# Kernel tuning notes

Hardware: AMD Instinct MI355X
Metric: run time of the kernel (lower is better)

The kernel has to match this reference:

```python
import jax, jax.numpy as jnp
import numpy as np

SCALE = 0.08838834764831845  # 1/sqrt(128)


def setup_inputs() -> dict:
    key = jax.random.key(0)
    k1, k2, k3, k4 = jax.random.split(key, 4)
    B, Sq, H, D = 1, 2048, 32, 128
    Skv, K = 4096, 256
    return {
        "q": jax.random.normal(k1, (B, Sq, H, D), jnp.float32),
        "kv": jax.random.normal(k2, (B, Skv, 2, D), jnp.float32),  # stacked K,V (MQA)
        "attn_sink": jax.random.normal(k3, (H,), jnp.float32),
        "topk_idxs": jax.random.randint(k4, (B, Sq, K), 0, Skv),
    }


def reference(q, kv, attn_sink, topk_idxs):
    # q:        [B, Sq, H, D]
    # kv:       [B, Skv, 2, D]  (index 0 = keys, 1 = values; shared across heads)
    # topk_idxs:[B, Sq, K]      per-query selected KV positions
    # attn_sink:[H]             per-head sink logit added to the softmax denominator
    B = q.shape[0]
    # Gather selected KV per query: [B, Sq, K, 2, D]
    gathered = kv[jnp.arange(B)[:, None, None], topk_idxs]
    k = gathered[..., 0, :]  # [B, Sq, K, D]
    v = gathered[..., 1, :]  # [B, Sq, K, D]

    scores = jnp.einsum("bqhd,bqkd->bqhk", q, k) * SCALE  # [B, Sq, H, K]
    sink = attn_sink[None, None, :, None]                  # [1, 1, H, 1]

    # Numerically stable softmax over K selected tokens + sink logit.
    m = jnp.maximum(jnp.max(scores, axis=-1, keepdims=True), sink)
    e = jnp.exp(scores - m)
    denom = jnp.sum(e, axis=-1, keepdims=True) + jnp.exp(sink - m)
    probs = e / denom                                      # sink absorbs leftover mass

    out = jnp.einsum("bqhk,bqkd->bqhd", probs, v)          # [B, Sq, H, D]
    return out
```

## Files before the change

### kernel.cpp

```cpp
#include <hip/hip_runtime.h>
#include <hip/hip_bf16.h>

#define SQ 2048
#define NH 32
#define DH 128
#define NK 256
#define SCALE 0.08838834764831845f
#define LOG2E 1.4426950408889634f

typedef __attribute__((ext_vector_type(8))) __bf16 bf16x8;
typedef __attribute__((ext_vector_type(4))) float floatx4;

#define QS_STRIDE 136
#define KS_STRIDE 136
#define VB_STRIDE 72
#define PB_STRIDE 264

#define OFF_KV   16896
#define OFF_TOPK 35328
#define OFF_SINK 36352
#define OFF_RED  36480
#define OFF_RED2 36992
#define SMEM_SZ  37504

__device__ __forceinline__ unsigned pk_bf16(float a, float b) {
  union { __hip_bfloat162 h2; unsigned u; } c;
  c.h2 = __float22bfloat162_rn(make_float2(a, b));
  return c.u;
}

__device__ __forceinline__ float fast_exp2(float x) {
#if __has_builtin(__builtin_amdgcn_exp2f)
  return __builtin_amdgcn_exp2f(x);
#else
  return exp2f(x);
#endif
}

template <int CTRL>
__device__ __forceinline__ float dpp_rot(float x) {
  int i = __builtin_bit_cast(int, x);
  i = __builtin_amdgcn_mov_dpp(i, CTRL, 0xF, 0xF, true);
  return __builtin_bit_cast(float, i);
}
#define RED16_MAX(v) { v = fmaxf(v, dpp_rot<0x121>(v)); v = fmaxf(v, dpp_rot<0x122>(v)); \
                       v = fmaxf(v, dpp_rot<0x124>(v)); v = fmaxf(v, dpp_rot<0x128>(v)); }
#define RED16_SUM(v) { v += dpp_rot<0x121>(v); v += dpp_rot<0x122>(v); \
                       v += dpp_rot<0x124>(v); v += dpp_rot<0x128>(v); }

__global__ __launch_bounds__(256) void kv_to_bf16(const float* __restrict__ kv,
                                                  unsigned short* __restrict__ kvb) {
  int i = blockIdx.x * 256 + threadIdx.x;
  float4 f = ((const float4*)kv)[i];
  uint2 o = { pk_bf16(f.x, f.y), pk_bf16(f.z, f.w) };
  ((uint2*)kvb)[i] = o;
}

struct KR { uint4 v[4]; };
struct VR { uint4 a, b, c, d; };

__device__ __forceinline__ KR k_load(const unsigned short* __restrict__ kvb,
                                     const int* __restrict__ tks, int c, int tid) {
  int r = tid >> 2, seg = tid & 3;
  int idx = tks[c * 64 + r];
  const uint4* p = (const uint4*)(kvb + (size_t)idx * 256 + seg * 32);
  KR k;
#pragma unroll
  for (int i = 0; i < 4; i++) k.v[i] = p[i];
  return k;
}

__device__ __forceinline__ void k_write(unsigned short* kvbuf, const KR& k, int tid) {
  int r = tid >> 2, seg = tid & 3;
  uint4* d = (uint4*)&kvbuf[r * KS_STRIDE + seg * 32];
#pragma unroll
  for (int i = 0; i < 4; i++) d[i] = k.v[i];
}

__device__ __forceinline__ VR v_load(const unsigned short* __restrict__ kvb,
                                     const int* tks, int c, int tid) {
  int rg = tid & 15, dg = tid >> 4;
  int r0 = rg * 4, d0 = dg * 8;
  int4 i4 = *(const int4*)&tks[c * 64 + r0];
  VR v;
  v.a = *(const uint4*)(kvb + (size_t)i4.x * 256 + 128 + d0);
  v.b = *(const uint4*)(kvb + (size_t)i4.y * 256 + 128 + d0);
  v.c = *(const uint4*)(kvb + (size_t)i4.z * 256 + 128 + d0);
  v.d = *(const uint4*)(kvb + (size_t)i4.w * 256 + 128 + d0);
  return v;
}

__device__ __forceinline__ void v_write(unsigned short* kvbuf, const VR& v, int tid) {
  int rg = tid & 15, dg = tid >> 4;
  int r0 = rg * 4, d0 = dg * 8;
  const unsigned* pa = (const unsigned*)&v.a;
  const unsigned* pb = (const unsigned*)&v.b;
  const unsigned* pc = (const unsigned*)&v.c;
  const unsigned* pd = (const unsigned*)&v.d;
#pragma unroll
  for (int w = 0; w < 4; w++) {
    unsigned lo01 = __builtin_amdgcn_perm(pb[w], pa[w], 0x05040100u);
    unsigned lo23 = __builtin_amdgcn_perm(pd[w], pc[w], 0x05040100u);
    unsigned hi01 = __builtin_amdgcn_perm(pb[w], pa[w], 0x07060302u);
    unsigned hi23 = __builtin_amdgcn_perm(pd[w], pc[w], 0x07060302u);
    uint2 lo = { lo01, lo23 }, hi = { hi01, hi23 };
    *(uint2*)&kvbuf[(d0 + 2 * w) * VB_STRIDE + r0] = lo;
    *(uint2*)&kvbuf[(d0 + 2 * w + 1) * VB_STRIDE + r0] = hi;
  }
}

__device__ __forceinline__ void gemm1(const unsigned short* kvbuf,
                                      const bf16x8 af[2][4], int nrow, int quad,
                                      floatx4& a0, floatx4& a1) {
  a0 = (floatx4){0.f, 0.f, 0.f, 0.f};
  a1 = (floatx4){0.f, 0.f, 0.f, 0.f};
#pragma unroll
  for (int ks = 0; ks < 4; ks++) {
    bf16x8 b = *(const bf16x8*)&kvbuf[nrow * KS_STRIDE + ks * 32 + quad * 8];
    a0 = __builtin_amdgcn_mfma_f32_16x16x32_bf16(af[0][ks], b, a0, 0, 0, 0);
    a1 = __builtin_amdgcn_mfma_f32_16x16x32_bf16(af[1][ks], b, a1, 0, 0, 0);
  }
}

__device__ __forceinline__ void pv_chunk(const unsigned short* pbuf,
                                         const unsigned short* kvbuf, int c,
                                         int wave, int quad, int l16,
                                         floatx4 oacc[2][2]) {
#pragma unroll
  for (int ks = 0; ks < 2; ks++) {
    int kof = c * 64 + ks * 32 + quad * 8;
    bf16x8 a0 = *(const bf16x8*)&pbuf[l16 * PB_STRIDE + kof];
    bf16x8 a1 = *(const bf16x8*)&pbuf[(16 + l16) * PB_STRIDE + kof];
    int kl = ks * 32 + quad * 8;
    bf16x8 b0 = *(const bf16x8*)&kvbuf[(wave * 32 + l16) * VB_STRIDE + kl];
    bf16x8 b1 = *(const bf16x8*)&kvbuf[(wave * 32 + 16 + l16) * VB_STRIDE + kl];
    oacc[0][0] = __builtin_amdgcn_mfma_f32_16x16x32_bf16(a0, b0, oacc[0][0], 0, 0, 0);
    oacc[0][1] = __builtin_amdgcn_mfma_f32_16x16x32_bf16(a0, b1, oacc[0][1], 0, 0, 0);
    oacc[1][0] = __builtin_amdgcn_mfma_f32_16x16x32_bf16(a1, b0, oacc[1][0], 0, 0, 0);
    oacc[1][1] = __builtin_amdgcn_mfma_f32_16x16x32_bf16(a1, b1, oacc[1][1], 0, 0, 0);
  }
}

__global__ __launch_bounds__(256, 4) void sparse_attn_kernel(
    const float* __restrict__ q, const unsigned short* __restrict__ kvb,
    const float* __restrict__ sink, const int* __restrict__ topk,
    float* __restrict__ out) {
  __shared__ __align__(16) char smem[SMEM_SZ];
  unsigned short* qs    = (unsigned short*)smem;
  unsigned short* pbuf  = (unsigned short*)smem;
  unsigned short* kvbuf = (unsigned short*)(smem + OFF_KV);
  int*   topk_s = (int*)(smem + OFF_TOPK);
  float* sink_s = (float*)(smem + OFF_SINK);
  float* red    = (float*)(smem + OFF_RED);
  float* red2   = (float*)(smem + OFF_RED2);

  const int tid = threadIdx.x;
  const int s = blockIdx.x;
  const int wave = tid >> 6;
  const int lane = tid & 63;
  const int quad = lane >> 4;
  const int l16 = lane & 15;
  const int* tkg = topk + (size_t)s * NK;

  topk_s[tid] = tkg[tid];
  if (tid < 32) sink_s[tid] = sink[tid] * LOG2E;
  {
    int r = tid >> 2, seg = tid & 3;
    int idx = tkg[r];
    const uint4* p = (const uint4*)(kvb + (size_t)idx * 256 + seg * 32);
    uint4* d = (uint4*)&kvbuf[r * KS_STRIDE + seg * 32];
#pragma unroll
    for (int i = 0; i < 4; i++) d[i] = p[i];
  }
  {
    const float QSC = SCALE * LOG2E;
    const float* qp = q + (size_t)s * (NH * DH);
    int h = tid >> 3, d0 = (tid & 7) * 16;
    const float4* src = (const float4*)(qp + h * DH + d0);
    float4 f0 = src[0], f1 = src[1], f2 = src[2], f3 = src[3];
    uint4 o0 = { pk_bf16(f0.x * QSC, f0.y * QSC), pk_bf16(f0.z * QSC, f0.w * QSC),
                 pk_bf16(f1.x * QSC, f1.y * QSC), pk_bf16(f1.z * QSC, f1.w * QSC) };
    uint4 o1 = { pk_bf16(f2.x * QSC, f2.y * QSC), pk_bf16(f2.z * QSC, f2.w * QSC),
                 pk_bf16(f3.x * QSC, f3.y * QSC), pk_bf16(f3.z * QSC, f3.w * QSC) };
    *(uint4*)&qs[h * QS_STRIDE + d0] = o0;
    *(uint4*)&qs[h * QS_STRIDE + d0 + 8] = o1;
  }
  KR k1 = k_load(kvb, tkg, 1, tid);
  __syncthreads();

  bf16x8 afrag[2][4];
#pragma unroll
  for (int mt = 0; mt < 2; mt++)
#pragma unroll
    for (int ks = 0; ks < 4; ks++)
      afrag[mt][ks] =
          *(const bf16x8*)&qs[(mt * 16 + l16) * QS_STRIDE + ks * 32 + quad * 8];

  const int nrow = wave * 16 + l16;

  floatx4 sc[4][2];
  gemm1(kvbuf, afrag, nrow, quad, sc[0][0], sc[0][1]);
  __syncthreads();
  k_write(kvbuf, k1, tid);
  KR k2 = k_load(kvb, topk_s, 2, tid);
  __syncthreads();

  gemm1(kvbuf, afrag, nrow, quad, sc[1][0], sc[1][1]);
  __syncthreads();
  k_write(kvbuf, k2, tid);
  KR k3 = k_load(kvb, topk_s, 3, tid);
  __syncthreads();

  gemm1(kvbuf, afrag, nrow, quad, sc[2][0], sc[2][1]);
  __syncthreads();
  k_write(kvbuf, k3, tid);
  VR v0 = v_load(kvb, topk_s, 0, tid);
  __syncthreads();

  gemm1(kvbuf, afrag, nrow, quad, sc[3][0], sc[3][1]);
  __syncthreads();
  v_write(kvbuf, v0, tid);
  VR v1 = v_load(kvb, topk_s, 1, tid);

  float mh[2][4];
#pragma unroll
  for (int mt = 0; mt < 2; mt++)
#pragma unroll
    for (int r = 0; r < 4; r++) {
      float v = fmaxf(fmaxf(sc[0][mt][r], sc[1][mt][r]),
                      fmaxf(sc[2][mt][r], sc[3][mt][r]));
      RED16_MAX(v);
      mh[mt][r] = v;
    }
  if (l16 == 0) {
#pragma unroll
    for (int mt = 0; mt < 2; mt++)
#pragma unroll
      for (int r = 0; r < 4; r++)
        red[wave * 32 + mt * 16 + quad * 4 + r] = mh[mt][r];
  }
  __syncthreads();
#pragma unroll
  for (int mt = 0; mt < 2; mt++)
#pragma unroll
    for (int r = 0; r < 4; r++) {
      int h = mt * 16 + quad * 4 + r;
      float v = sink_s[h];
#pragma unroll
      for (int w = 0; w < 4; w++) v = fmaxf(v, red[w * 32 + h]);
      mh[mt][r] = v;
    }
  float ps[2][4];
#pragma unroll
  for (int mt = 0; mt < 2; mt++)
#pragma unroll
    for (int r = 0; r < 4; r++) {
      float acc = 0.f;
#pragma unroll
      for (int c = 0; c < 4; c++) {
        float e = fast_exp2(sc[c][mt][r] - mh[mt][r]);
        sc[c][mt][r] = e;
        acc += e;
      }
      RED16_SUM(acc);
      ps[mt][r] = acc;
    }
  if (l16 == 0) {
#pragma unroll
    for (int mt = 0; mt < 2; mt++)
#pragma unroll
      for (int r = 0; r < 4; r++)
        red2[wave * 32 + mt * 16 + quad * 4 + r] = ps[mt][r];
  }
  __syncthreads();
  float inv[2][4];
#pragma unroll
  for (int mt = 0; mt < 2; mt++)
#pragma unroll
    for (int r = 0; r < 4; r++) {
      int h = mt * 16 + quad * 4 + r;
      float dd = fast_exp2(sink_s[h] - mh[mt][r]);
#pragma unroll
      for (int w = 0; w < 4; w++) dd += red2[w * 32 + h];
      inv[mt][r] = 1.0f / dd;
    }
#pragma unroll
  for (int c = 0; c < 4; c++)
#pragma unroll
    for (int mt = 0; mt < 2; mt++) {
      int col = c * 64 + wave * 16 + l16;
      unsigned short* pb = &pbuf[(mt * 16 + quad * 4) * PB_STRIDE + col];
      unsigned p01 = pk_bf16(sc[c][mt][0], sc[c][mt][1]);
      unsigned p23 = pk_bf16(sc[c][mt][2], sc[c][mt][3]);
      pb[0] = (unsigned short)p01;
      pb[PB_STRIDE] = (unsigned short)(p01 >> 16);
      pb[2 * PB_STRIDE] = (unsigned short)p23;
      pb[3 * PB_STRIDE] = (unsigned short)(p23 >> 16);
    }
  __syncthreads();

  floatx4 oacc[2][2];
#pragma unroll
  for (int mt = 0; mt < 2; mt++)
#pragma unroll
    for (int nt = 0; nt < 2; nt++)
      oacc[mt][nt] = (floatx4){0.f, 0.f, 0.f, 0.f};

  pv_chunk(pbuf, kvbuf, 0, wave, quad, l16, oacc);
  __syncthreads();
  v_write(kvbuf, v1, tid);
  VR v2 = v_load(kvb, topk_s, 2, tid);
  __syncthreads();

  pv_chunk(pbuf, kvbuf, 1, wave, quad, l16, oacc);
  __syncthreads();
  v_write(kvbuf, v2, tid);
  VR v3 = v_load(kvb, topk_s, 3, tid);
  __syncthreads();

  pv_chunk(pbuf, kvbuf, 2, wave, quad, l16, oacc);
  __syncthreads();
  v_write(kvbuf, v3, tid);
  __syncthreads();

  pv_chunk(pbuf, kvbuf, 3, wave, quad, l16, oacc);

  {
    float* op = out + (size_t)s * (NH * DH);
#pragma unroll
    for (int mt = 0; mt < 2; mt++)
#pragma unroll
      for (int nt = 0; nt < 2; nt++)
#pragma unroll
        for (int r4 = 0; r4 < 4; r4++) {
          int h = mt * 16 + quad * 4 + r4;
          int d = wave * 32 + nt * 16 + l16;
          op[h * DH + d] = oacc[mt][nt][r4] * inv[mt][r4];
        }
  }
}

extern "C" void kernel_launch(void* const* d_in, const int* in_sizes, int n_in,
                              void* d_out, int out_size, void* d_ws, size_t ws_size,
                              hipStream_t stream) {
  (void)in_sizes; (void)n_in; (void)out_size; (void)ws_size;
  const float* q    = (const float*)d_in[0];
  const float* kv   = (const float*)d_in[1];
  const float* sink = (const float*)d_in[2];
  const int*   topk = (const int*)d_in[3];
  float* out = (float*)d_out;
  unsigned short* kvb = (unsigned short*)d_ws;

  kv_to_bf16<<<dim3(1024), dim3(256), 0, stream>>>(kv, kvb);
  sparse_attn_kernel<<<dim3(SQ), dim3(256), 0, stream>>>(q, kvb, sink, topk, out);
}
```

Before: 113.4 us.

## Load K and Q MFMA fragments directly from global, drop LDS staging for QK

```diff
diff --git a/kernel.cpp b/kernel.cpp
--- a/kernel.cpp
+++ b/kernel.cpp
@@ -11,17 +11,14 @@
 typedef __attribute__((ext_vector_type(8))) __bf16 bf16x8;
 typedef __attribute__((ext_vector_type(4))) float floatx4;
 
-#define QS_STRIDE 136
-#define KS_STRIDE 136
 #define VB_STRIDE 72
 #define PB_STRIDE 264
 
-#define OFF_KV   16896
-#define OFF_TOPK 35328
-#define OFF_SINK 36352
-#define OFF_RED  36480
-#define OFF_RED2 36992
-#define SMEM_SZ  37504
+#define OFF_VB   16896
+#define OFF_SINK 35328
+#define OFF_RED  35456
+#define OFF_RED2 35968
+#define SMEM_SZ  36480
 
 __device__ __forceinline__ unsigned pk_bf16(float a, float b) {
   union { __hip_bfloat162 h2; unsigned u; } c;
@@ -56,32 +53,13 @@
   ((uint2*)kvb)[i] = o;
 }
 
-struct KR { uint4 v[4]; };
 struct VR { uint4 a, b, c, d; };
 
-__device__ __forceinline__ KR k_load(const unsigned short* __restrict__ kvb,
-                                     const int* __restrict__ tks, int c, int tid) {
-  int r = tid >> 2, seg = tid & 3;
-  int idx = tks[c * 64 + r];
-  const uint4* p = (const uint4*)(kvb + (size_t)idx * 256 + seg * 32);
-  KR k;
-#pragma unroll
-  for (int i = 0; i < 4; i++) k.v[i] = p[i];
-  return k;
-}
-
-__device__ __forceinline__ void k_write(unsigned short* kvbuf, const KR& k, int tid) {
-  int r = tid >> 2, seg = tid & 3;
-  uint4* d = (uint4*)&kvbuf[r * KS_STRIDE + seg * 32];
-#pragma unroll
-  for (int i = 0; i < 4; i++) d[i] = k.v[i];
-}
-
-__device__ __forceinline__ VR v_load(const unsigned short* __restrict__ kvb,
-                                     const int* tks, int c, int tid) {
+__device__ __forceinline__ VR v_load_g(const unsigned short* __restrict__ kvb,
+                                       const int* __restrict__ tkg, int c, int tid) {
   int rg = tid & 15, dg = tid >> 4;
   int r0 = rg * 4, d0 = dg * 8;
-  int4 i4 = *(const int4*)&tks[c * 64 + r0];
+  int4 i4 = *(const int4*)(tkg + c * 64 + r0);
   VR v;
   v.a = *(const uint4*)(kvb + (size_t)i4.x * 256 + 128 + d0);
   v.b = *(const uint4*)(kvb + (size_t)i4.y * 256 + 128 + d0);
@@ -90,7 +68,7 @@
   return v;
 }
 
-__device__ __forceinline__ void v_write(unsigned short* kvbuf, const VR& v, int tid) {
+__device__ __forceinline__ void v_write(unsigned short* vbuf, const VR& v, int tid) {
   int rg = tid & 15, dg = tid >> 4;
   int r0 = rg * 4, d0 = dg * 8;
   const unsigned* pa = (const unsigned*)&v.a;
@@ -104,26 +82,13 @@
     unsigned hi01 = __builtin_amdgcn_perm(pb[w], pa[w], 0x07060302u);
     unsigned hi23 = __builtin_amdgcn_perm(pd[w], pc[w], 0x07060302u);
     uint2 lo = { lo01, lo23 }, hi = { hi01, hi23 };
-    *(uint2*)&kvbuf[(d0 + 2 * w) * VB_STRIDE + r0] = lo;
-    *(uint2*)&kvbuf[(d0 + 2 * w + 1) * VB_STRIDE + r0] = hi;
-  }
-}
-
-__device__ __forceinline__ void gemm1(const unsigned short* kvbuf,
-                                      const bf16x8 af[2][4], int nrow, int quad,
-                                      floatx4& a0, floatx4& a1) {
-  a0 = (floatx4){0.f, 0.f, 0.f, 0.f};
-  a1 = (floatx4){0.f, 0.f, 0.f, 0.f};
-#pragma unroll
-  for (int ks = 0; ks < 4; ks++) {
-    bf16x8 b = *(const bf16x8*)&kvbuf[nrow * KS_STRIDE + ks * 32 + quad * 8];
-    a0 = __builtin_amdgcn_mfma_f32_16x16x32_bf16(af[0][ks], b, a0, 0, 0, 0);
-    a1 = __builtin_amdgcn_mfma_f32_16x16x32_bf16(af[1][ks], b, a1, 0, 0, 0);
+    *(uint2*)&vbuf[(d0 + 2 * w) * VB_STRIDE + r0] = lo;
+    *(uint2*)&vbuf[(d0 + 2 * w + 1) * VB_STRIDE + r0] = hi;
   }
 }
 
 __device__ __forceinline__ void pv_chunk(const unsigned short* pbuf,
-                                         const unsigned short* kvbuf, int c,
+                                         const unsigned short* vbuf, int c,
                                          int wave, int quad, int l16,
                                          floatx4 oacc[2][2]) {
 #pragma unroll
@@ -132,8 +97,8 @@
     bf16x8 a0 = *(const bf16x8*)&pbuf[l16 * PB_STRIDE + kof];
     bf16x8 a1 = *(const bf16x8*)&pbuf[(16 + l16) * PB_STRIDE + kof];
     int kl = ks * 32 + quad * 8;
-    bf16x8 b0 = *(const bf16x8*)&kvbuf[(wave * 32 + l16) * VB_STRIDE + kl];
-    bf16x8 b1 = *(const bf16x8*)&kvbuf[(wave * 32 + 16 + l16) * VB_STRIDE + kl];
+    bf16x8 b0 = *(const bf16x8*)&vbuf[(wave * 32 + l16) * VB_STRIDE + kl];
+    bf16x8 b1 = *(const bf16x8*)&vbuf[(wave * 32 + 16 + l16) * VB_STRIDE + kl];
     oacc[0][0] = __builtin_amdgcn_mfma_f32_16x16x32_bf16(a0, b0, oacc[0][0], 0, 0, 0);
     oacc[0][1] = __builtin_amdgcn_mfma_f32_16x16x32_bf16(a0, b1, oacc[0][1], 0, 0, 0);
     oacc[1][0] = __builtin_amdgcn_mfma_f32_16x16x32_bf16(a1, b0, oacc[1][0], 0, 0, 0);
@@ -146,10 +111,8 @@
     const float* __restrict__ sink, const int* __restrict__ topk,
     float* __restrict__ out) {
   __shared__ __align__(16) char smem[SMEM_SZ];
-  unsigned short* qs    = (unsigned short*)smem;
-  unsigned short* pbuf  = (unsigned short*)smem;
-  unsigned short* kvbuf = (unsigned short*)(smem + OFF_KV);
-  int*   topk_s = (int*)(smem + OFF_TOPK);
+  unsigned short* pbuf = (unsigned short*)smem;
+  unsigned short* vbuf = (unsigned short*)(smem + OFF_VB);
   float* sink_s = (float*)(smem + OFF_SINK);
   float* red    = (float*)(smem + OFF_RED);
   float* red2   = (float*)(smem + OFF_RED2);
@@ -161,66 +124,53 @@
   const int quad = lane >> 4;
   const int l16 = lane & 15;
   const int* tkg = topk + (size_t)s * NK;
-
-  topk_s[tid] = tkg[tid];
+  const float QSC = SCALE * LOG2E;
+
   if (tid < 32) sink_s[tid] = sink[tid] * LOG2E;
-  {
-    int r = tid >> 2, seg = tid & 3;
-    int idx = tkg[r];
-    const uint4* p = (const uint4*)(kvb + (size_t)idx * 256 + seg * 32);
-    uint4* d = (uint4*)&kvbuf[r * KS_STRIDE + seg * 32];
-#pragma unroll
-    for (int i = 0; i < 4; i++) d[i] = p[i];
-  }
-  {
-    const float QSC = SCALE * LOG2E;
-    const float* qp = q + (size_t)s * (NH * DH);
-    int h = tid >> 3, d0 = (tid & 7) * 16;
-    const float4* src = (const float4*)(qp + h * DH + d0);
-    float4 f0 = src[0], f1 = src[1], f2 = src[2], f3 = src[3];
-    uint4 o0 = { pk_bf16(f0.x * QSC, f0.y * QSC), pk_bf16(f0.z * QSC, f0.w * QSC),
-                 pk_bf16(f1.x * QSC, f1.y * QSC), pk_bf16(f1.z * QSC, f1.w * QSC) };
-    uint4 o1 = { pk_bf16(f2.x * QSC, f2.y * QSC), pk_bf16(f2.z * QSC, f2.w * QSC),
-                 pk_bf16(f3.x * QSC, f3.y * QSC), pk_bf16(f3.z * QSC, f3.w * QSC) };
-    *(uint4*)&qs[h * QS_STRIDE + d0] = o0;
-    *(uint4*)&qs[h * QS_STRIDE + d0 + 8] = o1;
-  }
-  KR k1 = k_load(kvb, tkg, 1, tid);
-  __syncthreads();
+
+  int kidx[4];
+#pragma unroll
+  for (int c = 0; c < 4; c++) kidx[c] = tkg[c * 64 + wave * 16 + l16];
 
   bf16x8 afrag[2][4];
 #pragma unroll
   for (int mt = 0; mt < 2; mt++)
 #pragma unroll
-    for (int ks = 0; ks < 4; ks++)
-      afrag[mt][ks] =
-          *(const bf16x8*)&qs[(mt * 16 + l16) * QS_STRIDE + ks * 32 + quad * 8];
-
-  const int nrow = wave * 16 + l16;
+    for (int ks = 0; ks < 4; ks++) {
+      const float4* p = (const float4*)(q + (size_t)s * (NH * DH) +
+                                        (mt * 16 + l16) * DH + ks * 32 + quad * 8);
+      float4 f0 = p[0], f1 = p[1];
+      union { uint4 u; bf16x8 h; } cv;
+      cv.u = (uint4){ pk_bf16(f0.x, f0.y), pk_bf16(f0.z, f0.w),
+                      pk_bf16(f1.x, f1.y), pk_bf16(f1.z, f1.w) };
+      afrag[mt][ks] = cv.h;
+    }
 
   floatx4 sc[4][2];
-  gemm1(kvbuf, afrag, nrow, quad, sc[0][0], sc[0][1]);
-  __syncthreads();
-  k_write(kvbuf, k1, tid);
-  KR k2 = k_load(kvb, topk_s, 2, tid);
-  __syncthreads();
-
-  gemm1(kvbuf, afrag, nrow, quad, sc[1][0], sc[1][1]);
-  __syncthreads();
-  k_write(kvbuf, k2, tid);
-  KR k3 = k_load(kvb, topk_s, 3, tid);
-  __syncthreads();
-
-  gemm1(kvbuf, afrag, nrow, quad, sc[2][0], sc[2][1]);
-  __syncthreads();
-  k_write(kvbuf, k3, tid);
-  VR v0 = v_load(kvb, topk_s, 0, tid);
-  __syncthreads();
-
-  gemm1(kvbuf, afrag, nrow, quad, sc[3][0], sc[3][1]);
-  __syncthreads();
-  v_write(kvbuf, v0, tid);
-  VR v1 = v_load(kvb, topk_s, 1, tid);
+  bf16x8 bk[2][4];
+#pragma unroll
+  for (int ks = 0; ks < 4; ks++)
+    bk[0][ks] = *(const bf16x8*)(kvb + (size_t)kidx[0] * 256 + ks * 32 + quad * 8);
+#pragma unroll
+  for (int c = 0; c < 4; c++) {
+    if (c < 3) {
+#pragma unroll
+      for (int ks = 0; ks < 4; ks++)
+        bk[(c + 1) & 1][ks] =
+            *(const bf16x8*)(kvb + (size_t)kidx[c + 1] * 256 + ks * 32 + quad * 8);
+    }
+    floatx4 a0 = {0.f, 0.f, 0.f, 0.f};
+    floatx4 a1 = {0.f, 0.f, 0.f, 0.f};
+#pragma unroll
+    for (int ks = 0; ks < 4; ks++) {
+      a0 = __builtin_amdgcn_mfma_f32_16x16x32_bf16(afrag[0][ks], bk[c & 1][ks], a0, 0, 0, 0);
+      a1 = __builtin_amdgcn_mfma_f32_16x16x32_bf16(afrag[1][ks], bk[c & 1][ks], a1, 0, 0, 0);
+    }
+    sc[c][0] = a0;
+    sc[c][1] = a1;
+  }
+
+  VR v0 = v_load_g(kvb, tkg, 0, tid);
 
   float mh[2][4];
 #pragma unroll
@@ -240,15 +190,17 @@
         red[wave * 32 + mt * 16 + quad * 4 + r] = mh[mt][r];
   }
   __syncthreads();
+  v_write(vbuf, v0, tid);
+  VR v1 = v_load_g(kvb, tkg, 1, tid);
 #pragma unroll
   for (int mt = 0; mt < 2; mt++)
 #pragma unroll
     for (int r = 0; r < 4; r++) {
       int h = mt * 16 + quad * 4 + r;
-      float v = sink_s[h];
-#pragma unroll
-      for (int w = 0; w < 4; w++) v = fmaxf(v, red[w * 32 + h]);
-      mh[mt][r] = v;
+      float v = red[h];
+#pragma unroll
+      for (int w = 1; w < 4; w++) v = fmaxf(v, red[w * 32 + h]);
+      mh[mt][r] = fmaxf(v * QSC, sink_s[h]);
     }
   float ps[2][4];
 #pragma unroll
@@ -258,7 +210,7 @@
       float acc = 0.f;
 #pragma unroll
       for (int c = 0; c < 4; c++) {
-        float e = fast_exp2(sc[c][mt][r] - mh[mt][r]);
+        float e = fast_exp2(fmaf(sc[c][mt][r], QSC, -mh[mt][r]));
         sc[c][mt][r] = e;
         acc += e;
       }
@@ -306,24 +258,24 @@
     for (int nt = 0; nt < 2; nt++)
       oacc[mt][nt] = (floatx4){0.f, 0.f, 0.f, 0.f};
 
-  pv_chunk(pbuf, kvbuf, 0, wave, quad, l16, oacc);
-  __syncthreads();
-  v_write(kvbuf, v1, tid);
-  VR v2 = v_load(kvb, topk_s, 2, tid);
-  __syncthreads();
-
-  pv_chunk(pbuf, kvbuf, 1, wave, quad, l16, oacc);
-  __syncthreads();
-  v_write(kvbuf, v2, tid);
-  VR v3 = v_load(kvb, topk_s, 3, tid);
-  __syncthreads();
-
-  pv_chunk(pbuf, kvbuf, 2, wave, quad, l16, oacc);
-  __syncthreads();
-  v_write(kvbuf, v3, tid);
-  __syncthreads();
-
-  pv_chunk(pbuf, kvbuf, 3, wave, quad, l16, oacc);
+  pv_chunk(pbuf, vbuf, 0, wave, quad, l16, oacc);
+  __syncthreads();
+  v_write(vbuf, v1, tid);
+  VR v2 = v_load_g(kvb, tkg, 2, tid);
+  __syncthreads();
+
+  pv_chunk(pbuf, vbuf, 1, wave, quad, l16, oacc);
+  __syncthreads();
+  v_write(vbuf, v2, tid);
+  VR v3 = v_load_g(kvb, tkg, 3, tid);
+  __syncthreads();
+
+  pv_chunk(pbuf, vbuf, 2, wave, quad, l16, oacc);
+  __syncthreads();
+  v_write(vbuf, v3, tid);
+  __syncthreads();
+
+  pv_chunk(pbuf, vbuf, 3, wave, quad, l16, oacc);
 
   {
     float* op = out + (size_t)s * (NH * DH);
```

New measurement: 130.0 us. 1.15x slower.
